# Optimization experiments

Hardware: AMD Instinct MI355X
Metric: run time of the kernel (lower is better)

The kernel has to match this reference:

```python
import jax, jax.numpy as jnp
import numpy as np

NW1, L1 = 4096, 36
NW2, L2 = 1024, 100
D, NHEAD = 128, 8
HD = D // NHEAD
# alternating full / half-full windows -> exact token count
N1 = (NW1 // 2) * (L1 + L1 // 2)   # 110592
N2 = (NW2 // 2) * (L2 + L2 // 2)   # 76800
N = N1 + N2                        # 187392


def _build_group(nw, L, perm, start):
    """Prefix-valid windows: even windows full (L tokens), odd half (L//2)."""
    lens = np.where(np.arange(nw) % 2 == 0, L, L // 2)
    valid = np.arange(L)[None, :] < lens[:, None]          # [nw, L]
    inds = np.zeros((nw, L), np.int32)
    n = int(lens.sum())
    inds[valid] = perm[start:start + n]                    # row-major prefix fill
    return inds, ~valid, start + n


def setup_inputs() -> dict:
    rng = np.random.default_rng(0)
    perm = rng.permutation(N).astype(np.int32)
    inds1, mask1, ptr = _build_group(NW1, L1, perm, 0)
    inds2, mask2, ptr = _build_group(NW2, L2, perm, ptr)
    assert ptr == N
    ks = jax.random.split(jax.random.key(0), 7)
    scale = 1.0 / np.sqrt(D)
    return {
        "feat_2d": jax.random.normal(ks[0], (N, D), jnp.float32),
        "pos1": jax.random.normal(ks[1], (NW1, L1, D), jnp.float32),
        "pos2": jax.random.normal(ks[2], (NW2, L2, D), jnp.float32),
        "in_proj_w": jax.random.normal(ks[3], (3 * D, D), jnp.float32) * scale,
        "in_proj_b": jax.random.normal(ks[4], (3 * D,), jnp.float32) * 0.02,
        "out_proj_w": jax.random.normal(ks[5], (D, D), jnp.float32) * scale,
        "out_proj_b": jax.random.normal(ks[6], (D,), jnp.float32) * 0.02,
        "inds1": jnp.asarray(inds1),
        "inds2": jnp.asarray(inds2),
        "mask1": jnp.asarray(mask1),
        "mask2": jnp.asarray(mask2),
    }


def _mha(qk, v, pad_mask, Wi, bi, Wo, bo):
    """torch.nn.MultiheadAttention math (eval mode, dropout=0).
    qk, v: [nw, L, D]; pad_mask: [nw, L] True=padded key."""
    nw, L, _ = qk.shape
    q = (qk @ Wi[:D].T + bi[:D]).reshape(nw, L, NHEAD, HD)
    k = (qk @ Wi[D:2 * D].T + bi[D:2 * D]).reshape(nw, L, NHEAD, HD)
    vv = (v @ Wi[2 * D:].T + bi[2 * D:]).reshape(nw, L, NHEAD, HD)
    scores = jnp.einsum('nqhd,nkhd->nhqk', q, k) * (HD ** -0.5)
    scores = jnp.where(pad_mask[:, None, None, :],
                       jnp.finfo(scores.dtype).min, scores)
    attn = jax.nn.softmax(scores, axis=-1)
    out = jnp.einsum('nhqk,nkhd->nqhd', attn, vv).reshape(nw, L, D)
    return out @ Wo.T + bo


def reference(feat_2d, pos1, pos2, in_proj_w, in_proj_b, out_proj_w,
              out_proj_b, inds1, inds2, mask1, mask2):
    out = jnp.zeros_like(feat_2d)
    for inds, mask, pos in ((inds1, mask1, pos1), (inds2, mask2, pos2)):
        f = feat_2d[inds]                      # flat2window gather [nw, L, D]
        o = _mha(f + pos, f, mask,
                 in_proj_w, in_proj_b, out_proj_w, out_proj_b)
        o = o * (~mask)[..., None]             # zero padded slots
        out = out.at[inds.reshape(-1)].add(o.reshape(-1, D))  # window2flat
    return out
```

## Files before the change

### kernel.cpp

```cpp
#include <hip/hip_runtime.h>

typedef __attribute__((ext_vector_type(4))) float f32x4;
typedef __attribute__((ext_vector_type(8))) short short8;
typedef __attribute__((ext_vector_type(4))) short short4v;

#define MFMA_B16(a,b,c) __builtin_amdgcn_mfma_f32_16x16x32_bf16((a),(b),(c),0,0,0)

static __device__ __forceinline__ unsigned short f2bf(float x){
  unsigned int u = __float_as_uint(x);
  u += 0x7fffu + ((u >> 16) & 1u);
  return (unsigned short)(u >> 16);
}

static __device__ __forceinline__ short8 pack8(f32x4 a, f32x4 b){
  short8 r;
  r[0]=(short)f2bf(a[0]); r[1]=(short)f2bf(a[1]); r[2]=(short)f2bf(a[2]); r[3]=(short)f2bf(a[3]);
  r[4]=(short)f2bf(b[0]); r[5]=(short)f2bf(b[1]); r[6]=(short)f2bf(b[2]); r[7]=(short)f2bf(b[3]);
  return r;
}

static __device__ __forceinline__ short8 xpose(const f32x4& X, int lane){
  const int c = lane & 15, q = lane >> 4;
  const int s0 = (q*32 + c) & 63, s1 = (q*32 + 16 + c) & 63;
  f32x4 lo, hi;
  #pragma unroll
  for (int r = 0; r < 4; ++r){ lo[r] = __shfl(X[r], s0); hi[r] = __shfl(X[r], s1); }
  return pack8(lo, hi);
}

__global__ void prep_w(const float* __restrict__ ipw, const float* __restrict__ opw,
                       unsigned short* __restrict__ wbf){
  int i = blockIdx.x * 256 + threadIdx.x;
  float v = (i < 384*128) ? ipw[i] : opw[i - 384*128];
  wbf[i] = f2bf(v);
}

#define STR 136

template<int TTP>
__global__ __launch_bounds__(256, 2)
void fused_attn(const float* __restrict__ feat,
                const float* __restrict__ pos,
                const int* __restrict__ inds,
                int LW,
                const unsigned short* __restrict__ wqkv,
                const unsigned short* __restrict__ wout,
                const float* __restrict__ ipb, const float* __restrict__ opb,
                float* __restrict__ out)
{
  constexpr int PSTR = 16*(TTP+1) + 8;
  extern __shared__ __align__(16) unsigned short smem[];
  unsigned short* sQK = smem;
  unsigned short* sF  = smem + 16*TTP*STR;
  unsigned short* sPb = smem + 2*16*TTP*STR;

  const int w = blockIdx.x;
  const int Lv = (w & 1) ? (LW >> 1) : LW;
  const int T  = (Lv + 15) >> 4;
  const long ibase = (long)w * LW;
  const int tid = threadIdx.x;
  const int wv = tid >> 6, lane = tid & 63, c = lane & 15, q = lane >> 4;
  const short8 Z8 = {0,0,0,0,0,0,0,0};
  const f32x4  Z4 = {0.f,0.f,0.f,0.f};

  {
    const int rg = tid >> 4, ch = tid & 15;
    #pragma unroll
    for (int s = 0; s < TTP; ++s){
      if (s < T){
        const int row = s*16 + rg;
        short8 fv = Z8, qv = Z8;
        if (row < Lv){
          const int tok = inds[ibase + row];
          const float* fr = feat + (long)tok*128 + ch*8;
          const float* pr = pos + (ibase + row)*128 + ch*8;
          f32x4 f0 = *(const f32x4*)fr, f1 = *(const f32x4*)(fr+4);
          f32x4 p0 = *(const f32x4*)pr, p1 = *(const f32x4*)(pr+4);
          fv = pack8(f0, f1); qv = pack8(f0+p0, f1+p1);
        }
        *(short8*)&sF [row*STR + ch*8] = fv;
        *(short8*)&sQK[row*STR + ch*8] = qv;
      }
    }
  }
  __syncthreads();

  unsigned short* Pb = sPb + wv*16*PSTR;
  if (T & 1){
    const short4v z4 = {0,0,0,0};
    *(short4v*)&Pb[c*PSTR + 16*T + 4*q] = z4;
  }
  short4v of[2][TTP];

  #pragma unroll
  for (int hh = 0; hh < 2; ++hh){
    const int h = wv*2 + hh;
    short8 bQ[4], bK[4], bV[4];
    const unsigned short* wr = wqkv + (h*16 + c)*128 + q*8;
    #pragma unroll
    for (int kk = 0; kk < 4; ++kk){
      bQ[kk] = *(const short8*)(wr + kk*32);
      bK[kk] = *(const short8*)(wr + kk*32 + 128*128);
      bV[kk] = *(const short8*)(wr + kk*32 + 2*128*128);
    }
    float bq_r[4], bk_r[4];
    #pragma unroll
    for (int r = 0; r < 4; ++r){
      bq_r[r] = ipb[h*16 + 4*q + r];
      bk_r[r] = ipb[128 + h*16 + 4*q + r];
    }
    const float bv_c = ipb[256 + h*16 + c];

    short8 qAf[TTP], kBf[TTP];
    f32x4 va[TTP];
    #pragma unroll
    for (int t = 0; t < TTP; ++t) va[t] = Z4;

    #pragma unroll
    for (int t = 0; t < TTP; ++t) if (t < T){
      f32x4 qt = Z4, kt = Z4, vt = Z4;
      #pragma unroll
      for (int kk = 0; kk < 4; ++kk){
        const short8 aQ = *(const short8*)&sQK[(16*t + c)*STR + kk*32 + q*8];
        const short8 aF = *(const short8*)&sF [(16*t + c)*STR + kk*32 + q*8];
        qt = MFMA_B16(bQ[kk], aQ, qt);
        kt = MFMA_B16(bK[kk], aQ, kt);
        vt = MFMA_B16(aF, bV[kk], vt);
      }
      #pragma unroll
      for (int r = 0; r < 4; ++r){
        qt[r] = (qt[r] + bq_r[r]) * 0.25f;
        kt[r] += bk_r[r];
        const int key = 16*t + 4*q + r;
        vt[r] = (key < Lv) ? (vt[r] + bv_c) : 0.f;
      }
      short8 tq8 = xpose(qt, lane);
      qAf[t] = (q < 2) ? tq8 : Z8;
      short8 tk8 = xpose(kt, lane);
      kBf[t] = (q < 2) ? tk8 : Z8;
      va[t] = vt;
    }

    short8 vBf[(TTP+1)/2];
    #pragma unroll
    for (int u = 0; u < (TTP+1)/2; ++u) if (u < ((T+1)>>1)){
      const int s0 = 32*(q & 1) + c, s1 = s0 + 16;
      f32x4 A0 = va[2*u];
      f32x4 A1 = (2*u+1 < TTP) ? va[2*u+1] : Z4;
      f32x4 lo, hi;
      #pragma unroll
      for (int r = 0; r < 4; ++r){
        float a0 = __shfl(A0[r], s0), a1 = __shfl(A1[r], s0);
        lo[r] = (q < 2) ? a0 : a1;
        float b0 = __shfl(A0[r], s1), b1 = __shfl(A1[r], s1);
        hi[r] = (q < 2) ? b0 : b1;
      }
      vBf[u] = pack8(lo, hi);
    }

    #pragma unroll
    for (int t = 0; t < TTP; ++t) if (t < T){
      f32x4 St[TTP];
      #pragma unroll
      for (int tk = 0; tk < TTP; ++tk) if (tk < T){
        St[tk] = MFMA_B16(kBf[tk], qAf[t], Z4);
        #pragma unroll
        for (int r = 0; r < 4; ++r){
          const int key = 16*tk + 4*q + r;
          if (key >= Lv) St[tk][r] = -1e30f;
        }
      }
      f32x4 mm = {-1e30f,-1e30f,-1e30f,-1e30f};
      #pragma unroll
      for (int tk = 0; tk < TTP; ++tk) if (tk < T){
        mm[0]=fmaxf(mm[0],St[tk][0]); mm[1]=fmaxf(mm[1],St[tk][1]);
        mm[2]=fmaxf(mm[2],St[tk][2]); mm[3]=fmaxf(mm[3],St[tk][3]);
      }
      float m = fmaxf(fmaxf(mm[0],mm[1]), fmaxf(mm[2],mm[3]));
      m = fmaxf(m, __shfl_xor(m, 16));
      m = fmaxf(m, __shfl_xor(m, 32));
      f32x4 ss = Z4;
      #pragma unroll
      for (int tk = 0; tk < TTP; ++tk) if (tk < T){
        #pragma unroll
        for (int r = 0; r < 4; ++r){
          float e = __expf(St[tk][r] - m);
          St[tk][r] = e; ss[r] += e;
        }
      }
      float sum = (ss[0]+ss[1]) + (ss[2]+ss[3]);
      sum += __shfl_xor(sum, 16);
      sum += __shfl_xor(sum, 32);
      const float inv = 1.0f / sum;
      #pragma unroll
      for (int tk = 0; tk < TTP; ++tk) if (tk < T){
        short4v p4;
        #pragma unroll
        for (int r = 0; r < 4; ++r) p4[r] = (short)f2bf(St[tk][r] * inv);
        *(short4v*)&Pb[c*PSTR + 16*tk + 4*q] = p4;
      }
      f32x4 o = Z4;
      #pragma unroll
      for (int u = 0; u < (TTP+1)/2; ++u) if (u < ((T+1)>>1)){
        const short8 ap = *(const short8*)&Pb[c*PSTR + 32*u + q*8];
        o = MFMA_B16(ap, vBf[u], o);
      }
      short4v ob;
      #pragma unroll
      for (int r = 0; r < 4; ++r) ob[r] = (short)f2bf(o[r]);
      of[hh][t] = ob;
    }
  }

  __syncthreads();
  #pragma unroll
  for (int hh = 0; hh < 2; ++hh){
    const int h = wv*2 + hh;
    #pragma unroll
    for (int t = 0; t < TTP; ++t) if (t < T){
      #pragma unroll
      for (int r = 0; r < 4; ++r)
        sF[(16*t + 4*q + r)*STR + h*16 + c] = (unsigned short)of[hh][t][r];
    }
  }
  __syncthreads();

  float bo_r[8];
  #pragma unroll
  for (int ct = 0; ct < 8; ++ct) bo_r[ct] = opb[ct*16 + c];
  #pragma unroll
  for (int ti = 0; ti < 2; ++ti){
    const int t = wv + ti*4;
    if (t < T){
      f32x4 acc[8];
      #pragma unroll
      for (int ct = 0; ct < 8; ++ct) acc[ct] = Z4;
      #pragma unroll
      for (int p = 0; p < 4; ++p){
        const short8 ao = *(const short8*)&sF[(16*t + c)*STR + p*32 + q*8];
        #pragma unroll
        for (int ct = 0; ct < 8; ++ct){
          const short8 bw = *(const short8*)&wout[(ct*16 + c)*128 + p*32 + q*8];
          acc[ct] = MFMA_B16(ao, bw, acc[ct]);
        }
      }
      #pragma unroll
      for (int r = 0; r < 4; ++r){
        const int l = 16*t + 4*q + r;
        if (l < Lv){
          const int tok = inds[ibase + l];
          float* orow = out + (long)tok*128;
          #pragma unroll
          for (int ct = 0; ct < 8; ++ct)
            orow[ct*16 + c] = acc[ct][r] + bo_r[ct];
        }
      }
    }
  }
}

extern "C" void kernel_launch(void* const* d_in, const int* in_sizes, int n_in,
                              void* d_out, int out_size, void* d_ws, size_t ws_size,
                              hipStream_t stream) {
  const float* feat = (const float*)d_in[0];
  const float* pos1 = (const float*)d_in[1];
  const float* pos2 = (const float*)d_in[2];
  const float* ipw  = (const float*)d_in[3];
  const float* ipb  = (const float*)d_in[4];
  const float* opw  = (const float*)d_in[5];
  const float* opb  = (const float*)d_in[6];
  const int*   inds1 = (const int*)d_in[7];
  const int*   inds2 = (const int*)d_in[8];
  float* out = (float*)d_out;
  unsigned short* wbf = (unsigned short*)d_ws;
  unsigned short* wob = wbf + 384*128;

  prep_w<<<dim3(256), dim3(256), 0, stream>>>(ipw, opw, wbf);

  {
    const int lds2 = (2*112*STR + 4*16*(16*8 + 8)) * 2;
    hipFuncSetAttribute((const void*)fused_attn<7>,
                        hipFuncAttributeMaxDynamicSharedMemorySize, lds2);
    fused_attn<7><<<dim3(1024), dim3(256), lds2, stream>>>(
        feat, pos2, inds2, 100, wbf, wob, ipb, opb, out);
  }
  {
    const int lds1 = (2*48*STR + 4*16*(16*4 + 8)) * 2;
    hipFuncSetAttribute((const void*)fused_attn<3>,
                        hipFuncAttributeMaxDynamicSharedMemorySize, lds1);
    fused_attn<3><<<dim3(4096), dim3(256), lds1, stream>>>(
        feat, pos1, inds1, 36, wbf, wob, ipb, opb, out);
  }
}
```

Before: 481.7 us.

## Add 8-wave one-head-per-wave kernel for the L=36 window group

Adds a specialised kernel for the 36-token windows that launches 512 threads (8 waves), with each wave owning one attention head. QKV projection B-fragments stay in registers, and the per-wave P buffer reuses the Q/K shared region. The out-projection is split across waves by token tile and column half. The goal is more parallelism per window and less LDS per block, in exchange for more barriers and more per-wave weight loads.

Result: slower. 502.4 us (+4.3%).

```diff
diff --git a/kernel.cpp b/kernel.cpp
--- a/kernel.cpp
+++ b/kernel.cpp
@@ -259,6 +259,223 @@
   }
 }
 
+#define TT3 3
+#define PSTR3 (16*(TT3+1) + 8)
+
+__global__ __launch_bounds__(512, 4)
+void fused_attn3_w8(const float* __restrict__ feat,
+                    const float* __restrict__ pos,
+                    const int* __restrict__ inds,
+                    const unsigned short* __restrict__ wqkv,
+                    const unsigned short* __restrict__ wout,
+                    const float* __restrict__ ipb, const float* __restrict__ opb,
+                    float* __restrict__ out)
+{
+  extern __shared__ __align__(16) unsigned short smem[];
+  unsigned short* sQK = smem;
+  unsigned short* sF  = smem + 48*STR;
+
+  const int w = blockIdx.x;
+  const int LW = 36;
+  const int Lv = (w & 1) ? 18 : 36;
+  const int T  = (Lv + 15) >> 4;
+  const long ibase = (long)w * LW;
+  const int tid = threadIdx.x;
+  const int wv = tid >> 6, lane = tid & 63, c = lane & 15, q = lane >> 4;
+  const short8 Z8 = {0,0,0,0,0,0,0,0};
+  const f32x4  Z4 = {0.f,0.f,0.f,0.f};
+
+  {
+    const int rg = tid >> 4, ch = tid & 15;
+    #pragma unroll
+    for (int s = 0; s < 2; ++s){
+      const int row = s*32 + rg;
+      if (row < 16*T){
+        short8 fv = Z8, qv = Z8;
+        if (row < Lv){
+          const int tok = inds[ibase + row];
+          const float* fr = feat + (long)tok*128 + ch*8;
+          const float* pr = pos + (ibase + row)*128 + ch*8;
+          f32x4 f0 = *(const f32x4*)fr, f1 = *(const f32x4*)(fr+4);
+          f32x4 p0 = *(const f32x4*)pr, p1 = *(const f32x4*)(pr+4);
+          fv = pack8(f0, f1); qv = pack8(f0+p0, f1+p1);
+        }
+        *(short8*)&sF [row*STR + ch*8] = fv;
+        *(short8*)&sQK[row*STR + ch*8] = qv;
+      }
+    }
+  }
+  __syncthreads();
+
+  const int h = wv;
+  short8 bQ[4], bK[4], bV[4];
+  const unsigned short* wr = wqkv + (h*16 + c)*128 + q*8;
+  #pragma unroll
+  for (int kk = 0; kk < 4; ++kk){
+    bQ[kk] = *(const short8*)(wr + kk*32);
+    bK[kk] = *(const short8*)(wr + kk*32 + 128*128);
+    bV[kk] = *(const short8*)(wr + kk*32 + 2*128*128);
+  }
+  float bq_r[4], bk_r[4];
+  #pragma unroll
+  for (int r = 0; r < 4; ++r){
+    bq_r[r] = ipb[h*16 + 4*q + r];
+    bk_r[r] = ipb[128 + h*16 + 4*q + r];
+  }
+  const float bv_c = ipb[256 + h*16 + c];
+
+  short8 qAf[TT3], kBf[TT3];
+  f32x4 va[TT3];
+  #pragma unroll
+  for (int t = 0; t < TT3; ++t) va[t] = Z4;
+
+  #pragma unroll
+  for (int t = 0; t < TT3; ++t) if (t < T){
+    f32x4 qt = Z4, kt = Z4, vt = Z4;
+    #pragma unroll
+    for (int kk = 0; kk < 4; ++kk){
+      const short8 aQ = *(const short8*)&sQK[(16*t + c)*STR + kk*32 + q*8];
+      const short8 aF = *(const short8*)&sF [(16*t + c)*STR + kk*32 + q*8];
+      qt = MFMA_B16(bQ[kk], aQ, qt);
+      kt = MFMA_B16(bK[kk], aQ, kt);
+      vt = MFMA_B16(aF, bV[kk], vt);
+    }
+    #pragma unroll
+    for (int r = 0; r < 4; ++r){
+      qt[r] = (qt[r] + bq_r[r]) * 0.25f;
+      kt[r] += bk_r[r];
+      const int key = 16*t + 4*q + r;
+      vt[r] = (key < Lv) ? (vt[r] + bv_c) : 0.f;
+    }
+    short8 tq8 = xpose(qt, lane);
+    qAf[t] = (q < 2) ? tq8 : Z8;
+    short8 tk8 = xpose(kt, lane);
+    kBf[t] = (q < 2) ? tk8 : Z8;
+    va[t] = vt;
+  }
+
+  short8 vBf[2];
+  #pragma unroll
+  for (int u = 0; u < 2; ++u) if (u < ((T+1)>>1)){
+    const int s0 = 32*(q & 1) + c, s1 = s0 + 16;
+    f32x4 A0 = va[2*u];
+    f32x4 A1 = (2*u+1 < TT3) ? va[2*u+1] : Z4;
+    f32x4 lo, hi;
+    #pragma unroll
+    for (int r = 0; r < 4; ++r){
+      float a0 = __shfl(A0[r], s0), a1 = __shfl(A1[r], s0);
+      lo[r] = (q < 2) ? a0 : a1;
+      float b0 = __shfl(A0[r], s1), b1 = __shfl(A1[r], s1);
+      hi[r] = (q < 2) ? b0 : b1;
+    }
+    vBf[u] = pack8(lo, hi);
+  }
+
+  __syncthreads();
+
+  unsigned short* Pb = smem + wv*16*PSTR3;
+  if (T & 1){
+    const short4v z4 = {0,0,0,0};
+    *(short4v*)&Pb[c*PSTR3 + 16*T + 4*q] = z4;
+  }
+  short4v of[TT3];
+
+  #pragma unroll
+  for (int t = 0; t < TT3; ++t) if (t < T){
+    f32x4 St[TT3];
+    #pragma unroll
+    for (int tk = 0; tk < TT3; ++tk) if (tk < T){
+      St[tk] = MFMA_B16(kBf[tk], qAf[t], Z4);
+      #pragma unroll
+      for (int r = 0; r < 4; ++r){
+        const int key = 16*tk + 4*q + r;
+        if (key >= Lv) St[tk][r] = -1e30f;
+      }
+    }
+    f32x4 mm = {-1e30f,-1e30f,-1e30f,-1e30f};
+    #pragma unroll
+    for (int tk = 0; tk < TT3; ++tk) if (tk < T){
+      mm[0]=fmaxf(mm[0],St[tk][0]); mm[1]=fmaxf(mm[1],St[tk][1]);
+      mm[2]=fmaxf(mm[2],St[tk][2]); mm[3]=fmaxf(mm[3],St[tk][3]);
+    }
+    float m = fmaxf(fmaxf(mm[0],mm[1]), fmaxf(mm[2],mm[3]));
+    m = fmaxf(m, __shfl_xor(m, 16));
+    m = fmaxf(m, __shfl_xor(m, 32));
+    f32x4 ss = Z4;
+    #pragma unroll
+    for (int tk = 0; tk < TT3; ++tk) if (tk < T){
+      #pragma unroll
+      for (int r = 0; r < 4; ++r){
+        float e = __expf(St[tk][r] - m);
+        St[tk][r] = e; ss[r] += e;
+      }
+    }
+    float sum = (ss[0]+ss[1]) + (ss[2]+ss[3]);
+    sum += __shfl_xor(sum, 16);
+    sum += __shfl_xor(sum, 32);
+    const float inv = 1.0f / sum;
+    #pragma unroll
+    for (int tk = 0; tk < TT3; ++tk) if (tk < T){
+      short4v p4;
+      #pragma unroll
+      for (int r = 0; r < 4; ++r) p4[r] = (short)f2bf(St[tk][r] * inv);
+      *(short4v*)&Pb[c*PSTR3 + 16*tk + 4*q] = p4;
+    }
+    f32x4 o = Z4;
+    #pragma unroll
+    for (int u = 0; u < 2; ++u) if (u < ((T+1)>>1)){
+      const short8 ap = *(const short8*)&Pb[c*PSTR3 + 32*u + q*8];
+      o = MFMA_B16(ap, vBf[u], o);
+    }
+    short4v ob;
+    #pragma unroll
+    for (int r = 0; r < 4; ++r) ob[r] = (short)f2bf(o[r]);
+    of[t] = ob;
+  }
+
+  __syncthreads();
+  #pragma unroll
+  for (int t = 0; t < TT3; ++t) if (t < T){
+    #pragma unroll
+    for (int r = 0; r < 4; ++r)
+      sF[(16*t + 4*q + r)*STR + h*16 + c] = (unsigned short)of[t][r];
+  }
+  __syncthreads();
+
+  {
+    const int t = wv >> 1;
+    const int cth = (wv & 1) * 4;
+    if (t < T){
+      float bo_r[4];
+      #pragma unroll
+      for (int cc = 0; cc < 4; ++cc) bo_r[cc] = opb[(cth + cc)*16 + c];
+      f32x4 acc[4];
+      #pragma unroll
+      for (int cc = 0; cc < 4; ++cc) acc[cc] = Z4;
+      #pragma unroll
+      for (int p = 0; p < 4; ++p){
+        const short8 ao = *(const short8*)&sF[(16*t + c)*STR + p*32 + q*8];
+        #pragma unroll
+        for (int cc = 0; cc < 4; ++cc){
+          const short8 bw = *(const short8*)&wout[((cth + cc)*16 + c)*128 + p*32 + q*8];
+          acc[cc] = MFMA_B16(ao, bw, acc[cc]);
+        }
+      }
+      #pragma unroll
+      for (int r = 0; r < 4; ++r){
+        const int l = 16*t + 4*q + r;
+        if (l < Lv){
+          const int tok = inds[ibase + l];
+          float* orow = out + (long)tok*128;
+          #pragma unroll
+          for (int cc = 0; cc < 4; ++cc)
+            orow[(cth + cc)*16 + c] = acc[cc][r] + bo_r[cc];
+        }
+      }
+    }
+  }
+}
+
 extern "C" void kernel_launch(void* const* d_in, const int* in_sizes, int n_in,
                               void* d_out, int out_size, void* d_ws, size_t ws_size,
                               hipStream_t stream) {
@@ -285,10 +502,10 @@
         feat, pos2, inds2, 100, wbf, wob, ipb, opb, out);
   }
   {
-    const int lds1 = (2*48*STR + 4*16*(16*4 + 8)) * 2;
-    hipFuncSetAttribute((const void*)fused_attn<3>,
+    const int lds1 = 2*48*STR*2;
+    hipFuncSetAttribute((const void*)fused_attn3_w8,
                         hipFuncAttributeMaxDynamicSharedMemorySize, lds1);
-    fused_attn<3><<<dim3(4096), dim3(256), lds1, stream>>>(
-        feat, pos1, inds1, 36, wbf, wob, ipb, opb, out);
-  }
-}
+    fused_attn3_w8<<<dim3(4096), dim3(512), lds1, stream>>>(
+        feat, pos1, inds1, wbf, wob, ipb, opb, out);
+  }
+}
```
